# Optimization experiments

Measured on AMD Instinct MI355X. Metric: run time of the kernel, lower is better.

The kernel has to match this reference:

```python
import jax, jax.numpy as jnp
import numpy as np

PATCH = (9, 7, 5, 3)
DIM = 64
HEAD_DIM = 64
HEADS = 8
HIDDEN = 8
DEPTH = 4
SCALE = (HEAD_DIM / HEADS) ** (-0.5)  # per-head dim = 8
EPS = 1e-5


def setup_inputs() -> dict:
    key = jax.random.key(0)
    ks = jax.random.split(key, 8)
    B = 4096
    x = jax.random.normal(ks[0], (B, PATCH[0] * PATCH[0], DIM), dtype=jnp.float32)
    w_qkv = jax.random.normal(ks[1], (DEPTH, DIM, 3 * HEAD_DIM), dtype=jnp.float32) * 0.05
    b_qkv = jnp.zeros((DEPTH, 3 * HEAD_DIM), dtype=jnp.float32)
    w_o = jax.random.normal(ks[2], (DEPTH, HEAD_DIM, DIM), dtype=jnp.float32) * 0.05
    b_o = jnp.zeros((DEPTH, DIM), dtype=jnp.float32)
    ln1_g = jnp.ones((DEPTH, DIM), dtype=jnp.float32)
    ln1_b = jnp.zeros((DEPTH, DIM), dtype=jnp.float32)
    ln2_g = jnp.ones((DEPTH, DIM), dtype=jnp.float32)
    ln2_b = jnp.zeros((DEPTH, DIM), dtype=jnp.float32)
    w1 = jax.random.normal(ks[3], (DEPTH, DIM, HIDDEN), dtype=jnp.float32) * 0.05
    b1 = jnp.zeros((DEPTH, HIDDEN), dtype=jnp.float32)
    w2 = jax.random.normal(ks[4], (DEPTH, HIDDEN, DIM), dtype=jnp.float32) * 0.05
    b2 = jnp.zeros((DEPTH, DIM), dtype=jnp.float32)
    return {"x": x, "w_qkv": w_qkv, "b_qkv": b_qkv, "w_o": w_o, "b_o": b_o,
            "ln1_g": ln1_g, "ln1_b": ln1_b, "ln2_g": ln2_g, "ln2_b": ln2_b,
            "w1": w1, "b1": b1, "w2": w2, "b2": b2}


def _layernorm(x, g, b):
    m = jnp.mean(x, axis=-1, keepdims=True)
    v = jnp.mean(jnp.square(x - m), axis=-1, keepdims=True)
    return (x - m) * jax.lax.rsqrt(v + EPS) * g + b


def reference(x, w_qkv, b_qkv, w_o, b_o, ln1_g, ln1_b, ln2_g, ln2_b, w1, b1, w2, b2):
    B = x.shape[0]
    for i in range(DEPTH):
        n = x.shape[1]
        # --- attention block (Residual(Layernorm(Encoder))) ---
        y = _layernorm(x, ln1_g[i], ln1_b[i])
        qkv = y @ w_qkv[i] + b_qkv[i]                       # [B, n, 3*HEAD_DIM]
        q, k, v = jnp.split(qkv, 3, axis=-1)
        dh = HEAD_DIM // HEADS                              # 8
        q = q.reshape(B, n, HEADS, dh)
        k = k.reshape(B, n, HEADS, dh)
        v = v.reshape(B, n, HEADS, dh)
        dots = jnp.einsum('bihd,bjhd->bhij', q, k) * SCALE  # [B, H, n, n]
        attn = jax.nn.softmax(dots, axis=-1)
        out = jnp.einsum('bhij,bjhd->bihd', attn, v).reshape(B, n, HEAD_DIM)
        out = out @ w_o[i] + b_o[i]
        x = x + out                                         # dropout = identity (eval)
        # --- feedforward block ---
        y = _layernorm(x, ln2_g[i], ln2_b[i])
        h = jax.nn.gelu(y @ w1[i] + b1[i], approximate=False)
        x = x + h @ w2[i] + b2[i]
        # --- spatial pooling / rearrange ---
        p = PATCH[i]
        xg = x.reshape(B, p, p, DIM)                        # 'b (h w) d -> b h w d'
        if i != DEPTH - 1:
            xg = xg[:, 1:-1, 1:-1, :]                       # crop pool_size=1
            x = xg.reshape(B, (p - 2) * (p - 2), DIM)
        else:
            x = jnp.transpose(xg, (0, 3, 1, 2))             # 'b h w d -> b d h w'
    return x  # [B, 64, 3, 3]
```

## Files before the change

### kernel.cpp

```cpp
#include <hip/hip_runtime.h>
#include <hip/hip_bf16.h>
#include <math.h>

#define NT 512

typedef __attribute__((ext_vector_type(8))) short short8v;
typedef __attribute__((ext_vector_type(4))) short short4v;
typedef __attribute__((ext_vector_type(4))) float f32x4;
typedef __attribute__((ext_vector_type(2))) unsigned uint2v;
typedef __attribute__((ext_vector_type(4))) unsigned uint4v;

__device__ __forceinline__ unsigned short f2bf(float x) {
    unsigned u = __float_as_uint(x);
    unsigned r = ((u >> 16) & 1u) + 0x7FFFu;
    return (unsigned short)((u + r) >> 16);
}
__device__ __forceinline__ unsigned pk2(float a, float b) {
    __hip_bfloat162 h = __float22bfloat162_rn(make_float2(a, b));
    unsigned r;
    __builtin_memcpy(&r, &h, sizeof(r));
    return r;
}
__device__ __forceinline__ short bf1(float a) {
    __hip_bfloat16 h = __float2bfloat16(a);
    short r;
    __builtin_memcpy(&r, &h, sizeof(r));
    return r;
}
__device__ __forceinline__ float exp2fast(float x) {
#if __has_builtin(__builtin_amdgcn_exp2f)
    return __builtin_amdgcn_exp2f(x);
#else
    return exp2f(x);
#endif
}
__device__ __forceinline__ float rcpfast(float x) {
#if __has_builtin(__builtin_amdgcn_rcpf)
    return __builtin_amdgcn_rcpf(x);
#else
    return 1.0f / x;
#endif
}
__device__ __forceinline__ float gelu_f(float x) {
    float x3 = x * x * x;
    float e = exp2fast(-2.3022079f * x - 0.1029432f * x3);
    return x * rcpfast(1.0f + e);
}
__device__ __forceinline__ f32x4 mfma32(short8v a, short8v b, f32x4 c) {
    return __builtin_amdgcn_mfma_f32_16x16x32_bf16(a, b, c, 0, 0, 0);
}
__device__ __forceinline__ f32x4 mfma16(short4v a, short4v b, f32x4 c) {
    return __builtin_amdgcn_mfma_f32_16x16x16bf16_1k(a, b, c, 0, 0, 0);
}

template<int M>
__device__ __forceinline__ void stats_tree(const f32x4* v, float& s1o, float& s2o) {
    float a[M], b[M];
    #pragma unroll
    for (int i = 0; i < M; ++i) {
        a[i] = (v[i][0] + v[i][1]) + (v[i][2] + v[i][3]);
        float q0 = v[i][0] * v[i][0], q1 = v[i][1] * v[i][1];
        float q2 = v[i][2] * v[i][2], q3 = v[i][3] * v[i][3];
        b[i] = (q0 + q1) + (q2 + q3);
    }
    #pragma unroll
    for (int s = 1; s < M; s *= 2)
        #pragma unroll
        for (int i = 0; i + s < M; i += 2 * s) { a[i] += a[i + s]; b[i] += b[i + s]; }
    s1o = a[0]; s2o = b[0];
}

#define WS_WO 49152
#define WS_W1 65536
#define WS_W2 69632
#define WS_TOT 71680

__global__ __launch_bounds__(256) void prep_kernel(
    const float* __restrict__ w_qkv, const float* __restrict__ w_o,
    const float* __restrict__ w1, const float* __restrict__ w2,
    short* __restrict__ ws)
{
    int idx = blockIdx.x * 256 + threadIdx.x;
    if (idx < WS_WO) {
        int l = idx / 12288, r = idx % 12288, c = r >> 6, d = r & 63;
        ws[idx] = (short)f2bf(w_qkv[l * 12288 + d * 192 + c]);
    } else if (idx < WS_W1) {
        int k = idx - WS_WO; int l = k / 4096, r = k % 4096, c = r >> 6, d = r & 63;
        ws[idx] = (short)f2bf(w_o[l * 4096 + d * 64 + c]);
    } else if (idx < WS_W2) {
        int k = idx - WS_W1; int l = k / 1024, r = k % 1024, j = r >> 6, d = r & 63;
        ws[idx] = (j < 8) ? (short)f2bf(w1[l * 512 + d * 8 + j]) : (short)0;
    } else if (idx < WS_TOT) {
        int k = idx - WS_W2; int l = k / 512, r = k % 512, c = r >> 3, j = r & 7;
        ws[idx] = (short)f2bf(w2[l * 512 + j * 64 + c]);
    }
}

template<int N, int P, int L, bool FIRST, bool LAST>
__device__ __forceinline__ void layer_fn(
    float* __restrict__ xs, short* __restrict__ ybuf, short* __restrict__ qbf,
    short* __restrict__ hb, const short* __restrict__ ws,
    const float* __restrict__ b_qkv, const float* __restrict__ b_o,
    const float* __restrict__ ln1_g, const float* __restrict__ ln1_b,
    const float* __restrict__ ln2_g, const float* __restrict__ ln2_b,
    const float* __restrict__ b1,    const float* __restrict__ b2,
    float* __restrict__ out, int b, int t)
{
    constexpr int Mt = (N + 15) / 16;
    constexpr float SCL2E = 0.51010905835f;
    const int wv = t >> 6, l = t & 63, lr = l & 15, lq = l >> 4;
    short8v zero8 = {};
    short4v zero4s = {};
    f32x4 zero4 = {0.f, 0.f, 0.f, 0.f};

    if (FIRST) {
        if (t < 64 * Mt) {
            const int token = t >> 2, part = t & 3, d0 = part * 16;
            short* yrow = ybuf + token * 72 + d0;
            if (token < N) {
                const int row = (token / P + L) * 9 + token % P + L;
                const float* xr = xs + row * 68 + d0;
                f32x4 v[4];
                #pragma unroll
                for (int k = 0; k < 4; ++k) v[k] = *(const f32x4*)(xr + 4 * k);
                float s1, s2;
                stats_tree<4>(v, s1, s2);
                s1 += __shfl_xor(s1, 1); s2 += __shfl_xor(s2, 1);
                s1 += __shfl_xor(s1, 2); s2 += __shfl_xor(s2, 2);
                const float m = s1 * 0.015625f;
                const float r = rsqrtf(s2 * 0.015625f - m * m + 1e-5f);
                uint4v w0, w1v;
                #pragma unroll
                for (int k = 0; k < 4; ++k) {
                    f32x4 g  = *(const f32x4*)&ln1_g[L * 64 + d0 + 4 * k];
                    f32x4 bb = *(const f32x4*)&ln1_b[L * 64 + d0 + 4 * k];
                    unsigned p0 = pk2((v[k][0]-m)*r*g[0]+bb[0], (v[k][1]-m)*r*g[1]+bb[1]);
                    unsigned p1 = pk2((v[k][2]-m)*r*g[2]+bb[2], (v[k][3]-m)*r*g[3]+bb[3]);
                    if (k == 0) { w0.x = p0; w0.y = p1; }
                    else if (k == 1) { w0.z = p0; w0.w = p1; }
                    else if (k == 2) { w1v.x = p0; w1v.y = p1; }
                    else { w1v.z = p0; w1v.w = p1; }
                }
                *(uint4v*)yrow = w0;
                *(uint4v*)(yrow + 8) = w1v;
            } else {
                uint4v z = {};
                *(uint4v*)yrow = z;
                *(uint4v*)(yrow + 8) = z;
            }
        }
        __syncthreads();
    }

    {
        const short* wqL = ws + L * 12288;
        for (int u = wv; u < Mt * 4; u += 8) {
            const int mt = u >> 2, ct = u & 3;
            const short* yr = &ybuf[(16 * mt + lr) * 72 + lq * 8];
            short8v y0 = *(const short8v*)yr, y1 = *(const short8v*)(yr + 32);
            const short* wr = &wqL[(16 * ct + lr) * 64 + lq * 8];
            short8v w0 = *(const short8v*)wr, w1 = *(const short8v*)(wr + 32);
            f32x4 acc = mfma32(w0, y0, zero4);
            acc = mfma32(w1, y1, acc);
            f32x4 bq = *(const f32x4*)&b_qkv[L * 192 + 16 * ct + lq * 4];
            const int i = 16 * mt + lr;
            unsigned p0 = pk2((acc[0]+bq[0])*SCL2E, (acc[1]+bq[1])*SCL2E);
            unsigned p1 = pk2((acc[2]+bq[2])*SCL2E, (acc[3]+bq[3])*SCL2E);
            unsigned* dst = (unsigned*)&qbf[i * 72 + 16 * ct + lq * 4];
            dst[0] = p0; dst[1] = p1;
        }
    }
    __syncthreads();

    {
        const int h = wv, a = h & 1, ct = h >> 1;
        const short* wqL = ws + L * 12288;

        short4v vf[Mt];
        {
            const short* wvr = &wqL[(128 + 16 * ct + lr) * 64 + lq * 8];
            short8v wv0 = *(const short8v*)wvr, wv1 = *(const short8v*)(wvr + 32);
            const float vbi = b_qkv[L * 192 + 128 + 16 * ct + lr];
            #pragma unroll
            for (int mt = 0; mt < Mt; ++mt) {
                const short* yr = &ybuf[(16 * mt + lr) * 72 + lq * 8];
                short8v y0 = *(const short8v*)yr, y1 = *(const short8v*)(yr + 32);
                f32x4 acc = mfma32(y0, wv0, zero4);
                acc = mfma32(y1, wv1, acc);
                uint2v u;
                u.x = pk2(acc[0] + vbi, acc[1] + vbi);
                u.y = pk2(acc[2] + vbi, acc[3] + vbi);
                vf[mt] = __builtin_bit_cast(short4v, u);
            }
        }
        const int srcl = lr + 32 * a + (l & 16);
        uint2v kf[Mt];
        {
            const short* wkr = &wqL[(64 + 16 * ct + lr) * 64 + lq * 8];
            short8v wk0 = *(const short8v*)wkr, wk1 = *(const short8v*)(wkr + 32);
            f32x4 kb = *(const f32x4*)&b_qkv[L * 192 + 64 + 16 * ct + lq * 4];
            #pragma unroll
            for (int mt = 0; mt < Mt; ++mt) {
                const short* yr = &ybuf[(16 * mt + lr) * 72 + lq * 8];
                short8v y0 = *(const short8v*)yr, y1 = *(const short8v*)(yr + 32);
                f32x4 acc = mfma32(wk0, y0, zero4);
                acc = mfma32(wk1, y1, acc);
                unsigned ka = pk2(acc[0] + kb[0], acc[1] + kb[1]);
                unsigned kc = pk2(acc[2] + kb[2], acc[3] + kb[3]);
                unsigned u0 = (unsigned)__shfl((int)ka, srcl);
                unsigned u1 = (unsigned)__shfl((int)kc, srcl);
                uint2v kv; kv.x = (l < 32) ? u0 : 0u; kv.y = (l < 32) ? u1 : 0u;
                kf[mt] = kv;
            }
        }
        for (int mt = 0; mt < Mt; ++mt) {
            short4v qv = zero4s;
            if (l < 32)
                qv = *(const short4v*)&qbf[(16 * mt + lr) * 72 + 8 * h + 4 * ((l >> 4) & 1)];
            float psA = 0.f, psB = 0.f;
            f32x4 po0 = zero4, po1 = zero4;
            #pragma unroll
            for (int jt = 0; jt < Mt; ++jt) {
                f32x4 s = mfma16(__builtin_bit_cast(short4v, kf[jt]), qv, zero4);
                float e0 = exp2fast(s[0]), e1 = exp2fast(s[1]);
                float e2 = exp2fast(s[2]), e3 = exp2fast(s[3]);
                if (jt == Mt - 1) {
                    const int j0 = 16 * jt + lq * 4;
                    e0 = (j0 + 0 < N) ? e0 : 0.f;
                    e1 = (j0 + 1 < N) ? e1 : 0.f;
                    e2 = (j0 + 2 < N) ? e2 : 0.f;
                    e3 = (j0 + 3 < N) ? e3 : 0.f;
                }
                psA += e0 + e1; psB += e2 + e3;
                uint2v pv; pv.x = pk2(e0, e1); pv.y = pk2(e2, e3);
                short4v bv = __builtin_bit_cast(short4v, pv);
                if (jt & 1) po1 = mfma16(vf[jt], bv, po1);
                else        po0 = mfma16(vf[jt], bv, po0);
            }
            float psum = psA + psB;
            float den = psum + __shfl_xor(psum, 16);
            den += __shfl_xor(den, 32);
            const float dinv = rcpfast(den);
            if ((lq >> 1) == a) {
                const int i = 16 * mt + lr;
                if (i < N) {
                    unsigned q0 = pk2((po0[0] + po1[0]) * dinv, (po0[1] + po1[1]) * dinv);
                    unsigned q1 = pk2((po0[2] + po1[2]) * dinv, (po0[3] + po1[3]) * dinv);
                    unsigned* dst = (unsigned*)&qbf[i * 72 + 8 * h + (lq & 1) * 4];
                    dst[0] = q0; dst[1] = q1;
                }
            }
        }
    }
    __syncthreads();

    {
        if (wv < Mt) {
            const int mt = wv;
            const int i = 16 * mt + lr;
            const bool iok = (i < N);
            const int xrow = iok ? (i / P + L) * 9 + (i % P) + L : 0;
            float* xp = xs + xrow * 68;
            const short* yr = &qbf[i * 72 + lq * 8];
            short8v y0 = *(const short8v*)yr;
            short8v y1 = *(const short8v*)(yr + 32);
            const short* woL = ws + WS_WO + L * 4096;
            f32x4 xv[4];
            #pragma unroll
            for (int ctp = 0; ctp < 4; ++ctp) {
                const short* wr = &woL[(16 * ctp + lr) * 64 + lq * 8];
                f32x4 acc = mfma32(*(const short8v*)wr, y0, zero4);
                acc = mfma32(*(const short8v*)(wr + 32), y1, acc);
                f32x4 bo = *(const f32x4*)&b_o[L * 64 + 16 * ctp + 4 * lq];
                f32x4 xc = zero4;
                if (iok) xc = *(const f32x4*)(xp + 16 * ctp + 4 * lq);
                #pragma unroll
                for (int rg = 0; rg < 4; ++rg) xc[rg] += acc[rg] + bo[rg];
                xv[ctp] = xc;
            }
            float s1, s2;
            stats_tree<4>(xv, s1, s2);
            s1 += __shfl_xor(s1, 16); s2 += __shfl_xor(s2, 16);
            s1 += __shfl_xor(s1, 32); s2 += __shfl_xor(s2, 32);
            const float m = s1 * 0.015625f;
            const float r = rsqrtf(s2 * 0.015625f - m * m + 1e-5f);
            unsigned* abw = (unsigned*)&qbf[i * 72];
            #pragma unroll
            for (int ctp = 0; ctp < 4; ++ctp) {
                f32x4 g  = *(const f32x4*)&ln2_g[L * 64 + 16 * ctp + 4 * lq];
                f32x4 bb = *(const f32x4*)&ln2_b[L * 64 + 16 * ctp + 4 * lq];
                abw[8 * ctp + 2 * lq]     = pk2((xv[ctp][0]-m)*r*g[0]+bb[0],
                                                (xv[ctp][1]-m)*r*g[1]+bb[1]);
                abw[8 * ctp + 2 * lq + 1] = pk2((xv[ctp][2]-m)*r*g[2]+bb[2],
                                                (xv[ctp][3]-m)*r*g[3]+bb[3]);
            }
            uint4v ua0 = *(const uint4v*)(abw + 4 * lq);
            uint4v ua1 = *(const uint4v*)(abw + 16 + 4 * lq);
            const short* w1L = ws + WS_W1 + L * 1024;
            short8v a10 = __builtin_bit_cast(short8v, ua0);
            short8v a11 = __builtin_bit_cast(short8v, ua1);
            short8v b10 = *(const short8v*)&w1L[lr * 64 + lq * 8];
            short8v b11 = *(const short8v*)&w1L[lr * 64 + lq * 8 + 32];
            f32x4 hA = mfma32(a10, b10, zero4);
            hA = mfma32(a11, b11, hA);
            if (lr < 8) {
                const float bg = b1[L * 8 + lr];
                #pragma unroll
                for (int rg = 0; rg < 4; ++rg)
                    hb[(16 * mt + 4 * lq + rg) * 8 + lr] = bf1(gelu_f(hA[rg] + bg));
            }
            short8v hbf = (lq == 0) ? *(const short8v*)&hb[(16 * mt + lr) * 8] : zero8;
            const short* w2L = ws + WS_W2 + L * 512;
            f32x4 xf[4];
            #pragma unroll
            for (int ctp = 0; ctp < 4; ++ctp) {
                short8v a2 = (lq == 0) ? *(const short8v*)&w2L[(16 * ctp + lr) * 8] : zero8;
                f32x4 dacc = mfma32(a2, hbf, zero4);
                f32x4 b2v = *(const f32x4*)&b2[L * 64 + 16 * ctp + 4 * lq];
                #pragma unroll
                for (int rg = 0; rg < 4; ++rg) xf[ctp][rg] = xv[ctp][rg] + dacc[rg] + b2v[rg];
                if (iok) *(f32x4*)(xp + 16 * ctp + 4 * lq) = xf[ctp];
            }
            if (!LAST) {
                float t1, t2;
                stats_tree<4>(xf, t1, t2);
                t1 += __shfl_xor(t1, 16); t2 += __shfl_xor(t2, 16);
                t1 += __shfl_xor(t1, 32); t2 += __shfl_xor(t2, 32);
                const float mn = t1 * 0.015625f;
                const float rn = rsqrtf(t2 * 0.015625f - mn * mn + 1e-5f);
                const int r_ = i / P, c_ = i % P;
                const bool vok = iok && r_ >= 1 && r_ <= P - 2 && c_ >= 1 && c_ <= P - 2;
                if (vok) {
                    const int j = (r_ - 1) * (P - 2) + (c_ - 1);
                    unsigned* yw = (unsigned*)&ybuf[j * 72];
                    #pragma unroll
                    for (int ctp = 0; ctp < 4; ++ctp) {
                        f32x4 g  = *(const f32x4*)&ln1_g[(L + 1) * 64 + 16 * ctp + 4 * lq];
                        f32x4 bb = *(const f32x4*)&ln1_b[(L + 1) * 64 + 16 * ctp + 4 * lq];
                        yw[8 * ctp + 2 * lq]     = pk2((xf[ctp][0]-mn)*rn*g[0]+bb[0],
                                                       (xf[ctp][1]-mn)*rn*g[1]+bb[1]);
                        yw[8 * ctp + 2 * lq + 1] = pk2((xf[ctp][2]-mn)*rn*g[2]+bb[2],
                                                       (xf[ctp][3]-mn)*rn*g[3]+bb[3]);
                    }
                }
            }
        } else if (!LAST && wv == Mt) {
            constexpr int Pn = P - 2, Nn = Pn * Pn, Mtn = (Nn + 15) / 16;
            constexpr int PadU = (16 * Mtn - Nn) * 36;
            unsigned* zb = (unsigned*)(ybuf + Nn * 72);
            for (int z = l; z < PadU; z += 64) zb[z] = 0;
        }
    }
    __syncthreads();

    if (LAST) {
        for (int idx = t; idx < 576; idx += NT) {
            const int d = idx / 9, rc = idx % 9;
            const int row = (rc / 3 + 3) * 9 + rc % 3 + 3;
            out[(size_t)b * 576 + idx] = xs[row * 68 + d];
        }
    }
}

__global__ __launch_bounds__(NT, 6) void vit_kernel(
    const float* __restrict__ x_in, const short* __restrict__ ws,
    const float* __restrict__ b_qkv, const float* __restrict__ b_o,
    const float* __restrict__ ln1_g, const float* __restrict__ ln1_b,
    const float* __restrict__ ln2_g, const float* __restrict__ ln2_b,
    const float* __restrict__ b1,    const float* __restrict__ b2,
    float* __restrict__ out)
{
    __shared__ __align__(16) float xs[81 * 68];
    __shared__ __align__(16) short ybuf[96 * 72];
    __shared__ __align__(16) short qbf[96 * 72];
    __shared__ __align__(16) short hb[96 * 8];

    const int b = blockIdx.x;
    const int t = threadIdx.x;

    const float* xin = x_in + (size_t)b * 5184;
    for (int q4 = t; q4 < 1296; q4 += NT) {
        const int i = q4 >> 4, dq = q4 & 15;
        *(f32x4*)&xs[i * 68 + dq * 4] = *(const f32x4*)&xin[i * 64 + dq * 4];
    }
    __syncthreads();

    layer_fn<81, 9, 0, true,  false>(xs, ybuf, qbf, hb, ws, b_qkv, b_o,
                                     ln1_g, ln1_b, ln2_g, ln2_b, b1, b2, out, b, t);
    layer_fn<49, 7, 1, false, false>(xs, ybuf, qbf, hb, ws, b_qkv, b_o,
                                     ln1_g, ln1_b, ln2_g, ln2_b, b1, b2, out, b, t);
    layer_fn<25, 5, 2, false, false>(xs, ybuf, qbf, hb, ws, b_qkv, b_o,
                                     ln1_g, ln1_b, ln2_g, ln2_b, b1, b2, out, b, t);
    layer_fn<9,  3, 3, false, true >(xs, ybuf, qbf, hb, ws, b_qkv, b_o,
                                     ln1_g, ln1_b, ln2_g, ln2_b, b1, b2, out, b, t);
}

extern "C" void kernel_launch(void* const* d_in, const int* in_sizes, int n_in,
                              void* d_out, int out_size, void* d_ws, size_t ws_size,
                              hipStream_t stream) {
    (void)n_in; (void)out_size; (void)ws_size;
    const float* x     = (const float*)d_in[0];
    const float* w_qkv = (const float*)d_in[1];
    const float* b_qkv = (const float*)d_in[2];
    const float* w_o   = (const float*)d_in[3];
    const float* b_o   = (const float*)d_in[4];
    const float* ln1_g = (const float*)d_in[5];
    const float* ln1_b = (const float*)d_in[6];
    const float* ln2_g = (const float*)d_in[7];
    const float* ln2_b = (const float*)d_in[8];
    const float* w1    = (const float*)d_in[9];
    const float* b1    = (const float*)d_in[10];
    const float* w2    = (const float*)d_in[11];
    const float* b2    = (const float*)d_in[12];
    short* ws = (short*)d_ws;

    prep_kernel<<<dim3((WS_TOT + 255) / 256), dim3(256), 0, stream>>>(w_qkv, w_o, w1, w2, ws);

    int B = in_sizes[0] / (81 * 64);
    vit_kernel<<<dim3(B), dim3(NT), 0, stream>>>(
        x, ws, b_qkv, b_o, ln1_g, ln1_b, ln2_g, ln2_b, b1, b2, (float*)d_out);
}
```

Before: 336.7 us.

## Compute Q per head in registers instead of staging through shared memory

```diff
diff --git a/kernel.cpp b/kernel.cpp
--- a/kernel.cpp
+++ b/kernel.cpp
@@ -110,7 +110,6 @@
     constexpr float SCL2E = 0.51010905835f;
     const int wv = t >> 6, l = t & 63, lr = l & 15, lq = l >> 4;
     short8v zero8 = {};
-    short4v zero4s = {};
     f32x4 zero4 = {0.f, 0.f, 0.f, 0.f};
 
     if (FIRST) {
@@ -153,70 +152,53 @@
     }
 
     {
+        const int h = wv, a = h & 1, ct = h >> 1;
+        const int srcl = lr + 32 * a + (l & 16);
         const short* wqL = ws + L * 12288;
-        for (int u = wv; u < Mt * 4; u += 8) {
-            const int mt = u >> 2, ct = u & 3;
+
+        const short* wqr = &wqL[(16 * ct + lr) * 64 + lq * 8];
+        short8v wq0 = *(const short8v*)wqr, wq1 = *(const short8v*)(wqr + 32);
+        f32x4 qb = *(const f32x4*)&b_qkv[L * 192 + 16 * ct + lq * 4];
+        const short* wkr = &wqL[(64 + 16 * ct + lr) * 64 + lq * 8];
+        short8v wk0 = *(const short8v*)wkr, wk1 = *(const short8v*)(wkr + 32);
+        f32x4 kb = *(const f32x4*)&b_qkv[L * 192 + 64 + 16 * ct + lq * 4];
+        const short* wvr = &wqL[(128 + 16 * ct + lr) * 64 + lq * 8];
+        short8v wv0 = *(const short8v*)wvr, wv1 = *(const short8v*)(wvr + 32);
+        const float vbi = b_qkv[L * 192 + 128 + 16 * ct + lr];
+
+        short4v vf[Mt];
+        uint2v kf[Mt];
+        #pragma unroll
+        for (int mt = 0; mt < Mt; ++mt) {
             const short* yr = &ybuf[(16 * mt + lr) * 72 + lq * 8];
             short8v y0 = *(const short8v*)yr, y1 = *(const short8v*)(yr + 32);
-            const short* wr = &wqL[(16 * ct + lr) * 64 + lq * 8];
-            short8v w0 = *(const short8v*)wr, w1 = *(const short8v*)(wr + 32);
-            f32x4 acc = mfma32(w0, y0, zero4);
-            acc = mfma32(w1, y1, acc);
-            f32x4 bq = *(const f32x4*)&b_qkv[L * 192 + 16 * ct + lq * 4];
-            const int i = 16 * mt + lr;
-            unsigned p0 = pk2((acc[0]+bq[0])*SCL2E, (acc[1]+bq[1])*SCL2E);
-            unsigned p1 = pk2((acc[2]+bq[2])*SCL2E, (acc[3]+bq[3])*SCL2E);
-            unsigned* dst = (unsigned*)&qbf[i * 72 + 16 * ct + lq * 4];
-            dst[0] = p0; dst[1] = p1;
-        }
-    }
-    __syncthreads();
-
-    {
-        const int h = wv, a = h & 1, ct = h >> 1;
-        const short* wqL = ws + L * 12288;
-
-        short4v vf[Mt];
-        {
-            const short* wvr = &wqL[(128 + 16 * ct + lr) * 64 + lq * 8];
-            short8v wv0 = *(const short8v*)wvr, wv1 = *(const short8v*)(wvr + 32);
-            const float vbi = b_qkv[L * 192 + 128 + 16 * ct + lr];
-            #pragma unroll
-            for (int mt = 0; mt < Mt; ++mt) {
-                const short* yr = &ybuf[(16 * mt + lr) * 72 + lq * 8];
-                short8v y0 = *(const short8v*)yr, y1 = *(const short8v*)(yr + 32);
-                f32x4 acc = mfma32(y0, wv0, zero4);
-                acc = mfma32(y1, wv1, acc);
-                uint2v u;
-                u.x = pk2(acc[0] + vbi, acc[1] + vbi);
-                u.y = pk2(acc[2] + vbi, acc[3] + vbi);
-                vf[mt] = __builtin_bit_cast(short4v, u);
-            }
-        }
-        const int srcl = lr + 32 * a + (l & 16);
-        uint2v kf[Mt];
-        {
-            const short* wkr = &wqL[(64 + 16 * ct + lr) * 64 + lq * 8];
-            short8v wk0 = *(const short8v*)wkr, wk1 = *(const short8v*)(wkr + 32);
-            f32x4 kb = *(const f32x4*)&b_qkv[L * 192 + 64 + 16 * ct + lq * 4];
-            #pragma unroll
-            for (int mt = 0; mt < Mt; ++mt) {
-                const short* yr = &ybuf[(16 * mt + lr) * 72 + lq * 8];
-                short8v y0 = *(const short8v*)yr, y1 = *(const short8v*)(yr + 32);
-                f32x4 acc = mfma32(wk0, y0, zero4);
-                acc = mfma32(wk1, y1, acc);
-                unsigned ka = pk2(acc[0] + kb[0], acc[1] + kb[1]);
-                unsigned kc = pk2(acc[2] + kb[2], acc[3] + kb[3]);
-                unsigned u0 = (unsigned)__shfl((int)ka, srcl);
-                unsigned u1 = (unsigned)__shfl((int)kc, srcl);
-                uint2v kv; kv.x = (l < 32) ? u0 : 0u; kv.y = (l < 32) ? u1 : 0u;
-                kf[mt] = kv;
-            }
+            f32x4 av = mfma32(y0, wv0, zero4);
+            av = mfma32(y1, wv1, av);
+            uint2v uv;
+            uv.x = pk2(av[0] + vbi, av[1] + vbi);
+            uv.y = pk2(av[2] + vbi, av[3] + vbi);
+            vf[mt] = __builtin_bit_cast(short4v, uv);
+            f32x4 ak = mfma32(wk0, y0, zero4);
+            ak = mfma32(wk1, y1, ak);
+            unsigned ka = pk2(ak[0] + kb[0], ak[1] + kb[1]);
+            unsigned kc = pk2(ak[2] + kb[2], ak[3] + kb[3]);
+            unsigned u0 = (unsigned)__shfl((int)ka, srcl);
+            unsigned u1 = (unsigned)__shfl((int)kc, srcl);
+            uint2v kv2; kv2.x = (l < 32) ? u0 : 0u; kv2.y = (l < 32) ? u1 : 0u;
+            kf[mt] = kv2;
         }
         for (int mt = 0; mt < Mt; ++mt) {
-            short4v qv = zero4s;
-            if (l < 32)
-                qv = *(const short4v*)&qbf[(16 * mt + lr) * 72 + 8 * h + 4 * ((l >> 4) & 1)];
+            const short* yr = &ybuf[(16 * mt + lr) * 72 + lq * 8];
+            short8v y0 = *(const short8v*)yr, y1 = *(const short8v*)(yr + 32);
+            f32x4 aq = mfma32(wq0, y0, zero4);
+            aq = mfma32(wq1, y1, aq);
+            unsigned qa = pk2((aq[0] + qb[0]) * SCL2E, (aq[1] + qb[1]) * SCL2E);
+            unsigned qc = pk2((aq[2] + qb[2]) * SCL2E, (aq[3] + qb[3]) * SCL2E);
+            unsigned uq0 = (unsigned)__shfl((int)qa, srcl);
+            unsigned uq1 = (unsigned)__shfl((int)qc, srcl);
+            uint2v qw; qw.x = (l < 32) ? uq0 : 0u; qw.y = (l < 32) ? uq1 : 0u;
+            short4v qv = __builtin_bit_cast(short4v, qw);
+
             float psA = 0.f, psB = 0.f;
             f32x4 po0 = zero4, po1 = zero4;
             #pragma unroll
@@ -378,6 +360,8 @@
     const int b = blockIdx.x;
     const int t = threadIdx.x;
 
+    for (int idx = t; idx < 96 * 72; idx += NT) qbf[idx] = 0;
+
     const float* xin = x_in + (size_t)b * 5184;
     for (int q4 = t; q4 < 1296; q4 += NT) {
         const int i = q4 >> 4, dq = q4 & 15;
```

Result: no change. 343.1 us (+1.9%).
